# Performance work log

Measured on AMD Instinct MI355X. Metric: run time of the kernel, lower is better.

The kernel has to match this reference:

```python
import jax, jax.numpy as jnp
import numpy as np

N_NEURONS = 100000
N_EDGES = 5000000
N_TYPES = 64
N_DM = 512
BATCH = 16
LAYER_NUMBER = 4  # number of connectome hops


def setup_inputs() -> dict:
    key = jax.random.key(0)
    ks = jax.random.split(key, 11)
    return {
        "x": jax.random.normal(ks[0], (N_NEURONS, BATCH), dtype=jnp.float32),
        "type_weight": jax.random.normal(ks[1], (N_TYPES,), dtype=jnp.float32),
        "type_bias": jax.random.normal(ks[2], (N_TYPES,), dtype=jnp.float32),
        # shared_weights = log1p(synapse counts) -> positive; use uniform
        "edge_weights": jax.random.uniform(ks[3], (N_EDGES,), dtype=jnp.float32),
        "dm_vals": jax.random.uniform(ks[4], (N_DM,), dtype=jnp.float32),
        "fc_w": jax.random.normal(ks[5], (1, N_DM), dtype=jnp.float32) * 0.04,
        "fc_b": jax.random.normal(ks[6], (1,), dtype=jnp.float32),
        "cell_type_indices": jax.random.randint(ks[7], (N_NEURONS,), 0, N_TYPES),
        "edge_rows": jax.random.randint(ks[8], (N_EDGES,), 0, N_NEURONS),
        "edge_cols": jax.random.randint(ks[9], (N_EDGES,), 0, N_NEURONS),
        "dm_cols": jax.random.randint(ks[10], (N_DM,), 0, N_NEURONS),
    }


def reference(x, type_weight, type_bias, edge_weights, dm_vals, fc_w, fc_b,
              cell_type_indices, edge_rows, edge_cols, dm_cols):
    # RetinaConnectionLayer: per-cell-type 1->1 linear (gathered scale + bias)
    h = x * type_weight[cell_type_indices][:, None] + type_bias[cell_type_indices][:, None]
    # AdultConnectome / SparseMatrixMul: repeated sparse COO matmul h = A @ h
    # with shared per-edge weights, applied layer_number times.
    for _ in range(LAYER_NUMBER):
        contrib = edge_weights[:, None] * h[edge_cols]          # [E, B] gather
        h = jax.ops.segment_sum(contrib, edge_rows, num_segments=N_NEURONS)
    # torch.sparse.mm(decision_making_tensor, h): row-selection sparse matrix
    y = dm_vals[:, None] * h[dm_cols]                           # [N_DM, B]
    # final_fc over the decision-neuron axis
    out = y.T @ fc_w.T + fc_b                                   # [B, 1]
    return out
```

## Files before the change

### kernel.cpp

```cpp
#include <hip/hip_runtime.h>

#define NN 100000
#define NE 5000000
#define NB 16
#define NDM 512

#define RPB 1024
#define NBUCKET 98
#define CAP 55296
#define CHUNK 8192
#define NCHUNK ((NE + CHUNK - 1) / CHUNK)
#define SUB 16
#define NWAVE 16

__global__ void setup(const float* __restrict__ dmv, const int* __restrict__ dmc,
                      const float* __restrict__ fcw,
                      float* __restrict__ u0, int* __restrict__ cursor) {
    int t = threadIdx.x;
    if (t < NDM) atomicAdd(&u0[dmc[t]], dmv[t] * fcw[t]);
    if (t < NBUCKET) cursor[t] = t * CAP;
}

__global__ void __launch_bounds__(1024, 8)
scatter_fused(const int* __restrict__ er, const int* __restrict__ ec,
              const float* __restrict__ ew,
              const float* __restrict__ u0, float* __restrict__ u1,
              int* __restrict__ cursor, int2* __restrict__ packed) {
    __shared__ int hist[NWAVE][NBUCKET];
    __shared__ int2 pval[CHUNK];
    __shared__ unsigned char sbk[CHUNK];
    __shared__ int lbloc[128];
    __shared__ int gbase[NBUCKET];
    __shared__ int ctot[NBUCKET];
    int tid = threadIdx.x;
    int wv = tid >> 6;
    for (int k = tid; k < NWAVE * NBUCKET; k += 1024) hist[k / NBUCKET][k % NBUCKET] = 0;
    __syncthreads();
    int base = blockIdx.x * CHUNK;
    int n = min(CHUNK, NE - base);
    int nq = n >> 2;
    const int4*   ec4 = (const int4*)(ec + base);
    const int4*   er4 = (const int4*)(er + base);
    const float4* ew4 = (const float4*)(ew + base);

    int2 ent[2][4];
    int  meta[2][4];
    #pragma unroll
    for (int g = 0; g < 2; ++g) {
        int k = tid + g * 1024;
        if (k < nq) {
            int4 c = ec4[k];
            int4 r = er4[k];
            float4 w = ew4[k];
            int cc[4] = {c.x, c.y, c.z, c.w};
            int rr[4] = {r.x, r.y, r.z, r.w};
            float ww[4] = {w.x, w.y, w.z, w.w};
            #pragma unroll
            for (int j = 0; j < 4; ++j) {
                int d = cc[j];
                int bk = d >> 10;
                int lp = atomicAdd(&hist[wv][bk], 1);
                ent[g][j] = make_int2(((d & 1023) << 17) | rr[j], __float_as_int(ww[j]));
                meta[g][j] = (lp << 7) | bk;
                float a = u0[rr[j]];
                if (a != 0.f) atomicAdd(&u1[d], ww[j] * a);
            }
        }
    }
    __syncthreads();
    if (tid < NBUCKET) {
        int c = 0;
        #pragma unroll
        for (int w = 0; w < NWAVE; ++w) c += hist[w][tid];
        ctot[tid] = c;
        gbase[tid] = c ? atomicAdd(&cursor[tid], c) : 0;
    }
    __syncthreads();
    if (tid < 128) lbloc[tid] = (tid < NBUCKET) ? ctot[tid] : 0;
    __syncthreads();
    for (int off = 1; off < 128; off <<= 1) {
        int v = 0;
        if (tid < 128 && tid >= off) v = lbloc[tid - off];
        __syncthreads();
        if (tid < 128) lbloc[tid] += v;
        __syncthreads();
    }
    if (tid < NBUCKET) {
        int lb = lbloc[tid] - ctot[tid];
        lbloc[tid] = lb;
        int c = lb;
        #pragma unroll
        for (int w = 0; w < NWAVE; ++w) {
            int t = hist[w][tid];
            hist[w][tid] = c;
            c += t;
        }
    }
    __syncthreads();
    #pragma unroll
    for (int g = 0; g < 2; ++g) {
        int k = tid + g * 1024;
        if (k < nq) {
            #pragma unroll
            for (int j = 0; j < 4; ++j) {
                int m = meta[g][j];
                int bk = m & 127;
                int pos = hist[wv][bk] + (m >> 7);
                pval[pos] = ent[g][j];
                sbk[pos] = (unsigned char)bk;
            }
        }
    }
    __syncthreads();
    for (int i = tid; i < n; i += 1024) {
        int bk = sbk[i];
        packed[gbase[bk] + (i - lbloc[bk])] = pval[i];
    }
}

__global__ void spmv_sorted(const int* __restrict__ cursor,
                            const int2* __restrict__ packed,
                            const float* __restrict__ wc, float* __restrict__ wn) {
    __shared__ float acc[RPB];
    int bucket = blockIdx.x >> 4;
    int sub = blockIdx.x & (SUB - 1);
    int t = threadIdx.x;
    #pragma unroll
    for (int k = 0; k < 4; ++k) acc[t + 256 * k] = 0.f;
    __syncthreads();
    int s = bucket * CAP;
    int e = cursor[bucket];
    int cnt = e - s;
    int slice = (cnt + SUB - 1) >> 4;
    int mys = s + sub * slice;
    int mye = min(mys + slice, e);
    int i = mys + t;
    for (; i + 768 < mye; i += 1024) {
        int2 p0 = packed[i];
        int2 p1 = packed[i + 256];
        int2 p2 = packed[i + 512];
        int2 p3 = packed[i + 768];
        float v0 = __int_as_float(p0.y) * wc[p0.x & 0x1FFFF];
        float v1 = __int_as_float(p1.y) * wc[p1.x & 0x1FFFF];
        float v2 = __int_as_float(p2.y) * wc[p2.x & 0x1FFFF];
        float v3 = __int_as_float(p3.y) * wc[p3.x & 0x1FFFF];
        if (v0 != 0.f) atomicAdd(&acc[p0.x >> 17], v0);
        if (v1 != 0.f) atomicAdd(&acc[p1.x >> 17], v1);
        if (v2 != 0.f) atomicAdd(&acc[p2.x >> 17], v2);
        if (v3 != 0.f) atomicAdd(&acc[p3.x >> 17], v3);
    }
    for (; i < mye; i += 256) {
        int2 p = packed[i];
        float v = __int_as_float(p.y) * wc[p.x & 0x1FFFF];
        if (v != 0.f) atomicAdd(&acc[p.x >> 17], v);
    }
    __syncthreads();
    #pragma unroll
    for (int k = 0; k < 4; ++k) {
        int row = bucket * RPB + t + 256 * k;
        float a = acc[t + 256 * k];
        if (a != 0.f && row < NN) atomicAdd(&wn[row], a);
    }
}

__global__ void final_dot(const float* __restrict__ x, const float* __restrict__ tw,
                          const float* __restrict__ tb, const int* __restrict__ ct,
                          const float* __restrict__ u,
                          float* __restrict__ acc_out) {
    __shared__ float s[512];
    __shared__ float sred[256][4];
    __shared__ float sbias[4];
    int tid = threadIdx.x;
    int base = blockIdx.x * 512;
    int nrows = min(512, NN - base);
    float accb = 0.f;
    for (int r = tid; r < nrows; r += 256) {
        int n = base + r;
        float un = u[n];
        int t = ct[n];
        s[r] = un * tw[t];
        accb = fmaf(un, tb[t], accb);
    }
    __syncthreads();
    float a0 = 0.f, a1 = 0.f, a2 = 0.f, a3 = 0.f;
    int j = (tid & 3) * 4;
    for (int r = tid >> 2; r < nrows; r += 64) {
        float4 xv = *(const float4*)&x[(size_t)(base + r) * NB + j];
        float sv = s[r];
        a0 = fmaf(sv, xv.x, a0);
        a1 = fmaf(sv, xv.y, a1);
        a2 = fmaf(sv, xv.z, a2);
        a3 = fmaf(sv, xv.w, a3);
    }
    sred[tid][0] = a0; sred[tid][1] = a1; sred[tid][2] = a2; sred[tid][3] = a3;
    for (int off = 32; off; off >>= 1) accb += __shfl_down(accb, off);
    if ((tid & 63) == 0) sbias[tid >> 6] = accb;
    __syncthreads();
    if (tid < 16) {
        int q = tid >> 2, k = tid & 3;
        float sum = 0.f;
        for (int i = 0; i < 64; ++i) sum += sred[q + 4 * i][k];
        atomicAdd(&acc_out[tid], sum);
    }
    if (tid == 16)
        atomicAdd(&acc_out[16], sbias[0] + sbias[1] + sbias[2] + sbias[3]);
}

__global__ void finalize(const float* __restrict__ acc, const float* __restrict__ fcb,
                         float* __restrict__ out) {
    int b = threadIdx.x;
    if (b < NB) out[b] = acc[b] + acc[16] + fcb[0];
}

extern "C" void kernel_launch(void* const* d_in, const int* in_sizes, int n_in,
                              void* d_out, int out_size, void* d_ws, size_t ws_size,
                              hipStream_t stream) {
    const float* x   = (const float*)d_in[0];
    const float* tw  = (const float*)d_in[1];
    const float* tb  = (const float*)d_in[2];
    const float* ew  = (const float*)d_in[3];
    const float* dmv = (const float*)d_in[4];
    const float* fcw = (const float*)d_in[5];
    const float* fcb = (const float*)d_in[6];
    const int* ct  = (const int*)d_in[7];
    const int* er  = (const int*)d_in[8];
    const int* ec  = (const int*)d_in[9];
    const int* dmc = (const int*)d_in[10];
    float* out = (float*)d_out;

    char* ws = (char*)d_ws;
    float* u   = (float*)ws;
    float* acc = u + 5 * (size_t)NN;
    size_t zero_bytes = (5 * (size_t)NN + 32) * 4;
    ws += zero_bytes;
    int* cursor = (int*)ws;         ws += 128 * 4;
    ws = (char*)(((uintptr_t)ws + 15) & ~(uintptr_t)15);
    int2* packed = (int2*)ws;

    hipMemsetAsync(u, 0, zero_bytes, stream);

    setup<<<1, 512, 0, stream>>>(dmv, dmc, fcw, u, cursor);

    scatter_fused<<<NCHUNK, 1024, 0, stream>>>(er, ec, ew, u, u + NN, cursor, packed);

    for (int l = 1; l < 4; ++l) {
        spmv_sorted<<<NBUCKET * SUB, 256, 0, stream>>>(cursor, packed,
                                                       u + (size_t)l * NN,
                                                       u + (size_t)(l + 1) * NN);
    }

    final_dot<<<(NN + 511) / 512, 256, 0, stream>>>(x, tw, tb, ct, u + 4 * (size_t)NN, acc);
    finalize<<<1, 64, 0, stream>>>(acc, fcb, out);
}
```

Before: 155.5 us.

## Vectorize sorted SpMV loads, duplicate LDS accumulators, per-bucket wave copy-out

In the scatter kernel, the per-element bucket byte array is removed, and the global write-out now runs per bucket, one wave per bucket, with contiguous copies. The sorted SpMV now loads two packed entries per thread as an int4. To keep those loads 16-byte aligned, the slice size is rounded up to an even count. Two LDS accumulator copies, split by wave parity, reduce atomic contention, and the copies are summed at flush. Alignment depends on the bucket base CAP being even and the packed buffer being 16-byte aligned. The per-bucket copy-out may leave waves idle on small buckets.

New measurement: 155.9 us. Within noise of the previous version (+0.3%).

```diff
diff --git a/kernel.cpp b/kernel.cpp
--- a/kernel.cpp
+++ b/kernel.cpp
@@ -28,7 +28,6 @@
               int* __restrict__ cursor, int2* __restrict__ packed) {
     __shared__ int hist[NWAVE][NBUCKET];
     __shared__ int2 pval[CHUNK];
-    __shared__ unsigned char sbk[CHUNK];
     __shared__ int lbloc[128];
     __shared__ int gbase[NBUCKET];
     __shared__ int ctot[NBUCKET];
@@ -105,60 +104,69 @@
             for (int j = 0; j < 4; ++j) {
                 int m = meta[g][j];
                 int bk = m & 127;
-                int pos = hist[wv][bk] + (m >> 7);
-                pval[pos] = ent[g][j];
-                sbk[pos] = (unsigned char)bk;
+                pval[hist[wv][bk] + (m >> 7)] = ent[g][j];
             }
         }
     }
     __syncthreads();
-    for (int i = tid; i < n; i += 1024) {
-        int bk = sbk[i];
-        packed[gbase[bk] + (i - lbloc[bk])] = pval[i];
+    int lane = tid & 63;
+    for (int b = wv; b < NBUCKET; b += NWAVE) {
+        int cnt = ctot[b];
+        int lb = lbloc[b];
+        int gb = gbase[b];
+        for (int j = lane; j < cnt; j += 64)
+            packed[gb + j] = pval[lb + j];
     }
 }
 
 __global__ void spmv_sorted(const int* __restrict__ cursor,
                             const int2* __restrict__ packed,
                             const float* __restrict__ wc, float* __restrict__ wn) {
-    __shared__ float acc[RPB];
+    __shared__ float acc[2][RPB];
     int bucket = blockIdx.x >> 4;
     int sub = blockIdx.x & (SUB - 1);
     int t = threadIdx.x;
-    #pragma unroll
-    for (int k = 0; k < 4; ++k) acc[t + 256 * k] = 0.f;
+    int cpy = (t >> 6) & 1;
+    #pragma unroll
+    for (int k = 0; k < 8; ++k) acc[k & 1][(k >> 1) * 256 + t] = 0.f;
     __syncthreads();
     int s = bucket * CAP;
     int e = cursor[bucket];
     int cnt = e - s;
-    int slice = (cnt + SUB - 1) >> 4;
+    int slice = (((cnt + SUB - 1) >> 4) + 1) & ~1;
     int mys = s + sub * slice;
     int mye = min(mys + slice, e);
-    int i = mys + t;
-    for (; i + 768 < mye; i += 1024) {
-        int2 p0 = packed[i];
-        int2 p1 = packed[i + 256];
-        int2 p2 = packed[i + 512];
-        int2 p3 = packed[i + 768];
-        float v0 = __int_as_float(p0.y) * wc[p0.x & 0x1FFFF];
-        float v1 = __int_as_float(p1.y) * wc[p1.x & 0x1FFFF];
-        float v2 = __int_as_float(p2.y) * wc[p2.x & 0x1FFFF];
-        float v3 = __int_as_float(p3.y) * wc[p3.x & 0x1FFFF];
-        if (v0 != 0.f) atomicAdd(&acc[p0.x >> 17], v0);
-        if (v1 != 0.f) atomicAdd(&acc[p1.x >> 17], v1);
-        if (v2 != 0.f) atomicAdd(&acc[p2.x >> 17], v2);
-        if (v3 != 0.f) atomicAdd(&acc[p3.x >> 17], v3);
-    }
-    for (; i < mye; i += 256) {
+    int i = mys + 2 * t;
+    for (; i + 513 < mye; i += 1024) {
+        int4 a = *(const int4*)&packed[i];
+        int4 b = *(const int4*)&packed[i + 512];
+        float v0 = __int_as_float(a.y) * wc[a.x & 0x1FFFF];
+        float v1 = __int_as_float(a.w) * wc[a.z & 0x1FFFF];
+        float v2 = __int_as_float(b.y) * wc[b.x & 0x1FFFF];
+        float v3 = __int_as_float(b.w) * wc[b.z & 0x1FFFF];
+        if (v0 != 0.f) atomicAdd(&acc[cpy][a.x >> 17], v0);
+        if (v1 != 0.f) atomicAdd(&acc[cpy][a.z >> 17], v1);
+        if (v2 != 0.f) atomicAdd(&acc[cpy][b.x >> 17], v2);
+        if (v3 != 0.f) atomicAdd(&acc[cpy][b.z >> 17], v3);
+    }
+    for (; i + 1 < mye; i += 512) {
+        int4 a = *(const int4*)&packed[i];
+        float v0 = __int_as_float(a.y) * wc[a.x & 0x1FFFF];
+        float v1 = __int_as_float(a.w) * wc[a.z & 0x1FFFF];
+        if (v0 != 0.f) atomicAdd(&acc[cpy][a.x >> 17], v0);
+        if (v1 != 0.f) atomicAdd(&acc[cpy][a.z >> 17], v1);
+    }
+    if (i < mye) {
         int2 p = packed[i];
         float v = __int_as_float(p.y) * wc[p.x & 0x1FFFF];
-        if (v != 0.f) atomicAdd(&acc[p.x >> 17], v);
+        if (v != 0.f) atomicAdd(&acc[cpy][p.x >> 17], v);
     }
     __syncthreads();
     #pragma unroll
     for (int k = 0; k < 4; ++k) {
-        int row = bucket * RPB + t + 256 * k;
-        float a = acc[t + 256 * k];
+        int r = t + 256 * k;
+        float a = acc[0][r] + acc[1][r];
+        int row = bucket * RPB + r;
         if (a != 0.f && row < NN) atomicAdd(&wn[row], a);
     }
 }
```
